# Optimization experiments

Hardware: AMD Instinct MI355X
Metric: run time of the kernel (lower is better)

The kernel has to match this reference:

```python
import jax, jax.numpy as jnp
import numpy as np


def setup_inputs() -> dict:
    key = jax.random.key(0)
    ks = jax.random.split(key, 4)
    B, T, C, L, DQ = 8, 2048, 256, 32, 512
    return {
        "vis_feats": jax.random.normal(ks[0], (B, T, C), dtype=jnp.float32),
        "query": jax.random.normal(ks[1], (B, L, DQ), dtype=jnp.float32),
        "W1": jax.random.normal(ks[2], (DQ, C), dtype=jnp.float32) / np.float32(np.sqrt(DQ)),
        "b1": jnp.zeros((C,), dtype=jnp.float32),
        "W2": jax.random.normal(ks[3], (DQ, C), dtype=jnp.float32) / np.float32(np.sqrt(DQ)),
        "b2": jnp.zeros((C,), dtype=jnp.float32),
        "window_size": 32,
        "num_chunks": 8,
    }


def reference(vis_feats, query, W1, b1, W2, b2, window_size, num_chunks):
    B, T, C = vis_feats.shape
    L = query.shape[1]
    # seq encoders (modeled as linear projections): [B, L, C]
    enc1 = query @ W1 + b1
    enc2 = query @ W2 + b2
    # clip-word similarity and per-clip word label: [B, T]
    sim = jnp.einsum("btc,blc->btl", vis_feats, enc1)
    clip_labels = jnp.argmax(sim, axis=2)
    NW = T - window_size + 1
    cic = window_size // num_chunks  # clips per chunk
    # sliding-window unfold indices: [NW, window_size]
    idx = jnp.arange(NW)[:, None] + jnp.arange(window_size)[None, :]
    vis_unf = vis_feats[:, idx, :]                      # [B, NW, W, C]
    lab_unf = clip_labels[:, idx].reshape(B, NW, num_chunks, cic)
    # majority vote per chunk == argmax of label histogram (ties -> smallest label,
    # matching np.bincount + np.argmax)
    counts = jax.nn.one_hot(lab_unf, L, dtype=jnp.int32).sum(axis=3)  # [B, NW, K, L]
    lbls = jnp.argmax(counts, axis=-1)                  # [B, NW, K]
    # adaptive_avg_pool3d (K, cic, C) -> (K, 1, C) == mean over clips-in-chunk
    pooled = vis_unf.reshape(B, NW, num_chunks, cic, C).mean(axis=3)  # [B, NW, K, C]
    # gather the majority-vote word encoding and modulate
    gathered = enc2[jnp.arange(B)[:, None, None], lbls]  # [B, NW, K, C]
    return gathered * pooled
```

## Files before the change

### kernel.cpp

```cpp
#include <hip/hip_runtime.h>
#include <hip/hip_bf16.h>

#define B   8
#define T   2048
#define C   256
#define L   32
#define DQ  512
#define NW  2017
#define NK  8
#define CIC 4
#define WT  32
#define SROWS (WT + (NK-1)*CIC)
#define LT  32

__global__ __launch_bounds__(256) void enc_kernel(
    const float* __restrict__ query, const float* __restrict__ W1,
    const float* __restrict__ b1, const float* __restrict__ W2,
    const float* __restrict__ b2, float* __restrict__ enc1,
    float* __restrict__ enc2) {
  const int b = blockIdx.y, lg = blockIdx.x;
  const int c = threadIdx.x;
  const float* q0 = query + ((size_t)b * L + lg * 4) * DQ;
  float a1[4] = {0.f, 0.f, 0.f, 0.f};
  float a2[4] = {0.f, 0.f, 0.f, 0.f};
#pragma unroll 8
  for (int d = 0; d < DQ; ++d) {
    const float w1 = W1[d * C + c];
    const float w2 = W2[d * C + c];
#pragma unroll
    for (int j = 0; j < 4; ++j) {
      const float qv = q0[j * DQ + d];
      a1[j] = fmaf(qv, w1, a1[j]);
      a2[j] = fmaf(qv, w2, a2[j]);
    }
  }
  const float bb1 = b1[c], bb2 = b2[c];
#pragma unroll
  for (int j = 0; j < 4; ++j) {
    const size_t off = ((size_t)b * L + lg * 4 + j) * C + c;
    enc1[off] = a1[j] + bb1;
    enc2[off] = a2[j] + bb2;
  }
}

__global__ __launch_bounds__(256) void label_kernel(
    const float* __restrict__ vis, const float* __restrict__ enc1,
    int* __restrict__ labels) {
  const int b = blockIdx.y;
  const int t0 = blockIdx.x * LT;
  const int tid = threadIdx.x;
  const int l = tid & 31;
  const int part = tid >> 5;
  __shared__ float4 raw[LT * (C / 4)];
  __shared__ alignas(16) float pacc[4][LT][36];

  float4 ef[8];
  {
    const float4* e1p = (const float4*)(enc1 + ((size_t)b * L + l) * C) + part * 8;
#pragma unroll
    for (int j = 0; j < 8; ++j) ef[j] = e1p[j];
  }
  const float4* vb = (const float4*)(vis + (size_t)b * T * C);
  for (int i = tid; i < LT * (C / 4); i += 256)
    raw[i] = vb[(size_t)(t0 + (i >> 6)) * (C / 4) + (i & 63)];
  __syncthreads();

  for (int t = 0; t < LT; ++t) {
    const float4* vr = &raw[t * (C / 4) + part * 8];
    float a = 0.f;
#pragma unroll
    for (int j = 0; j < 8; ++j) {
      const float4 v = vr[j];
      a = fmaf(v.x, ef[j].x, fmaf(v.y, ef[j].y, fmaf(v.z, ef[j].z, fmaf(v.w, ef[j].w, a))));
    }
    a += __shfl_down(a, 32);
    if (!(tid & 32)) pacc[tid >> 6][t][l] = a;
  }
  __syncthreads();

  if (tid < LT) {
    float4 s4[8];
#pragma unroll
    for (int j = 0; j < 8; ++j) s4[j] = make_float4(0.f, 0.f, 0.f, 0.f);
#pragma unroll
    for (int p = 0; p < 4; ++p) {
      const float4* pp = (const float4*)pacc[p][tid];
#pragma unroll
      for (int j = 0; j < 8; ++j) {
        s4[j].x += pp[j].x; s4[j].y += pp[j].y;
        s4[j].z += pp[j].z; s4[j].w += pp[j].w;
      }
    }
    float bv = -INFINITY;
    int bi = 0;
#pragma unroll
    for (int j = 0; j < 8; ++j) {
      if (s4[j].x > bv) { bv = s4[j].x; bi = 4 * j; }
      if (s4[j].y > bv) { bv = s4[j].y; bi = 4 * j + 1; }
      if (s4[j].z > bv) { bv = s4[j].z; bi = 4 * j + 2; }
      if (s4[j].w > bv) { bv = s4[j].w; bi = 4 * j + 3; }
    }
    labels[(size_t)b * T + t0 + tid] = bi;
  }
}

__global__ __launch_bounds__(256) void out_kernel(
    const float* __restrict__ vis, const float* __restrict__ enc2,
    const int* __restrict__ labels, float* __restrict__ out) {
  const int b = blockIdx.y;
  const int w0 = blockIdx.x * WT;
  const int tid = threadIdx.x;
  const int lane = tid & 63;
  const int wv = tid >> 6;
  __shared__ float4 S4[SROWS * (C / 4)];
  __shared__ int slbl[SROWS];

  int l0 = 0, l1 = 0, l2 = 0, l3 = 0;
  if (tid < SROWS) {
    const int* lb = labels + (size_t)b * T;
    const int t = w0 + tid;
#define LCL(tt) lb[(tt) > (T - 1) ? (T - 1) : (tt)]
    l0 = LCL(t); l1 = LCL(t + 1); l2 = LCL(t + 2); l3 = LCL(t + 3);
#undef LCL
  }

  const float4* vb = (const float4*)(vis + (size_t)b * T * C);
  float4 r[18];
  {
    const int s0 = wv * (SROWS / 4);
#pragma unroll
    for (int j = 0; j < 18; ++j) {
      int t = w0 + s0 + j;
      t = t > (T - 1) ? (T - 1) : t;
      r[j] = vb[(size_t)t * (C / 4) + lane];
    }
  }

  if (tid < SROWS) {
    const int c0 = 1 + (l0 == l1) + (l0 == l2) + (l0 == l3);
    const int c1 = 1 + (l1 == l0) + (l1 == l2) + (l1 == l3);
    const int c2 = 1 + (l2 == l0) + (l2 == l1) + (l2 == l3);
    const int c3 = 1 + (l3 == l0) + (l3 == l1) + (l3 == l2);
    int best = l0, bc = c0;
    if (c1 > bc || (c1 == bc && l1 < best)) { best = l1; bc = c1; }
    if (c2 > bc || (c2 == bc && l2 < best)) { best = l2; bc = c2; }
    if (c3 > bc || (c3 == bc && l3 < best)) { best = l3; bc = c3; }
    slbl[tid] = best;
  }

  {
    const int s0 = wv * (SROWS / 4);
#pragma unroll
    for (int s = 0; s < SROWS / 4; ++s) {
      float4 o;
      o.x = (r[s].x + r[s + 1].x + r[s + 2].x + r[s + 3].x) * 0.25f;
      o.y = (r[s].y + r[s + 1].y + r[s + 2].y + r[s + 3].y) * 0.25f;
      o.z = (r[s].z + r[s + 1].z + r[s + 2].z + r[s + 3].z) * 0.25f;
      o.w = (r[s].w + r[s + 1].w + r[s + 2].w + r[s + 3].w) * 0.25f;
      S4[(s0 + s) * (C / 4) + lane] = o;
    }
  }
  __syncthreads();

  const float4* e2b = (const float4*)(enc2 + (size_t)b * L * C);
  float4* outp = (float4*)out;
  const int wlim = (NW - w0) < WT ? (NW - w0) : WT;
#pragma unroll
  for (int kk = 0; kk < 2; ++kk) {
    const int k = wv + kk * 4;
#pragma unroll 4
    for (int w = 0; w < wlim; ++w) {
      const int s = w + CIC * k;
      const int lb = slbl[s];
      const float4 e = e2b[lb * (C / 4) + lane];
      const float4 sv = S4[s * (C / 4) + lane];
      float4 o;
      o.x = e.x * sv.x; o.y = e.y * sv.y; o.z = e.z * sv.z; o.w = e.w * sv.w;
      outp[(((size_t)b * NW + w0 + w) * NK + k) * (C / 4) + lane] = o;
    }
  }
}

extern "C" void kernel_launch(void* const* d_in, const int* in_sizes, int n_in,
                              void* d_out, int out_size, void* d_ws, size_t ws_size,
                              hipStream_t stream) {
  const float* vis   = (const float*)d_in[0];
  const float* query = (const float*)d_in[1];
  const float* W1    = (const float*)d_in[2];
  const float* b1    = (const float*)d_in[3];
  const float* W2    = (const float*)d_in[4];
  const float* b2    = (const float*)d_in[5];
  float* out = (float*)d_out;

  float* enc1 = (float*)d_ws;
  float* enc2 = enc1 + (size_t)B * L * C;
  int* labels = (int*)(enc2 + (size_t)B * L * C);

  enc_kernel<<<dim3(L / 4, B), 256, 0, stream>>>(query, W1, b1, W2, b2, enc1, enc2);
  label_kernel<<<dim3(T / LT, B), 256, 0, stream>>>(vis, enc1, labels);
  out_kernel<<<dim3((NW + WT - 1) / WT, B), 256, 0, stream>>>(vis, enc2, labels, out);
}
```

Measured before the change: 229.1 us.

## Split encoder projection over DQ into partial-sum blocks plus reduction kernel

```diff
diff --git a/kernel.cpp b/kernel.cpp
--- a/kernel.cpp
+++ b/kernel.cpp
@@ -12,34 +12,64 @@
 #define WT  32
 #define SROWS (WT + (NK-1)*CIC)
 #define LT  32
-
-__global__ __launch_bounds__(256) void enc_kernel(
+#define DS  4
+#define DSL (DQ / DS)
+#define PCHUNK (2 * B * L * C)
+
+__global__ __launch_bounds__(256) void enc_partial(
     const float* __restrict__ query, const float* __restrict__ W1,
-    const float* __restrict__ b1, const float* __restrict__ W2,
+    const float* __restrict__ W2, float* __restrict__ P) {
+  const int lg = blockIdx.x, b = blockIdx.y, ds = blockIdx.z;
+  const int c = threadIdx.x;
+  __shared__ float4 qs4[4][DSL / 4];
+
+  if (c < 4 * (DSL / 4)) {
+    const int j = c >> 5, g = c & 31;
+    qs4[j][g] = ((const float4*)(query + ((size_t)b * L + lg * 4 + j) * DQ + ds * DSL))[g];
+  }
+  __syncthreads();
+
+  float a1[4] = {0.f, 0.f, 0.f, 0.f};
+  float a2[4] = {0.f, 0.f, 0.f, 0.f};
+#pragma unroll 4
+  for (int g = 0; g < DSL / 4; ++g) {
+    const float4 q0 = qs4[0][g], q1 = qs4[1][g], q2 = qs4[2][g], q3 = qs4[3][g];
+    const float* wp1 = W1 + (size_t)(ds * DSL + 4 * g) * C + c;
+    const float* wp2 = W2 + (size_t)(ds * DSL + 4 * g) * C + c;
+    const float w10 = wp1[0], w11 = wp1[C], w12 = wp1[2 * C], w13 = wp1[3 * C];
+    const float w20 = wp2[0], w21 = wp2[C], w22 = wp2[2 * C], w23 = wp2[3 * C];
+    a1[0] = fmaf(q0.x, w10, fmaf(q0.y, w11, fmaf(q0.z, w12, fmaf(q0.w, w13, a1[0]))));
+    a1[1] = fmaf(q1.x, w10, fmaf(q1.y, w11, fmaf(q1.z, w12, fmaf(q1.w, w13, a1[1]))));
+    a1[2] = fmaf(q2.x, w10, fmaf(q2.y, w11, fmaf(q2.z, w12, fmaf(q2.w, w13, a1[2]))));
+    a1[3] = fmaf(q3.x, w10, fmaf(q3.y, w11, fmaf(q3.z, w12, fmaf(q3.w, w13, a1[3]))));
+    a2[0] = fmaf(q0.x, w20, fmaf(q0.y, w21, fmaf(q0.z, w22, fmaf(q0.w, w23, a2[0]))));
+    a2[1] = fmaf(q1.x, w20, fmaf(q1.y, w21, fmaf(q1.z, w22, fmaf(q1.w, w23, a2[1]))));
+    a2[2] = fmaf(q2.x, w20, fmaf(q2.y, w21, fmaf(q2.z, w22, fmaf(q2.w, w23, a2[2]))));
+    a2[3] = fmaf(q3.x, w20, fmaf(q3.y, w21, fmaf(q3.z, w22, fmaf(q3.w, w23, a2[3]))));
+  }
+
+#pragma unroll
+  for (int j = 0; j < 4; ++j) {
+    const size_t base = ((((size_t)ds * 2 + 0) * B + b) * 8 + lg) * 4 + j;
+    P[base * C + c] = a1[j];
+    P[(base + (size_t)B * 8 * 4) * C + c] = a2[j];
+  }
+}
+
+__global__ __launch_bounds__(256) void enc_reduce(
+    const float* __restrict__ P, const float* __restrict__ b1,
     const float* __restrict__ b2, float* __restrict__ enc1,
     float* __restrict__ enc2) {
-  const int b = blockIdx.y, lg = blockIdx.x;
-  const int c = threadIdx.x;
-  const float* q0 = query + ((size_t)b * L + lg * 4) * DQ;
-  float a1[4] = {0.f, 0.f, 0.f, 0.f};
-  float a2[4] = {0.f, 0.f, 0.f, 0.f};
-#pragma unroll 8
-  for (int d = 0; d < DQ; ++d) {
-    const float w1 = W1[d * C + c];
-    const float w2 = W2[d * C + c];
-#pragma unroll
-    for (int j = 0; j < 4; ++j) {
-      const float qv = q0[j * DQ + d];
-      a1[j] = fmaf(qv, w1, a1[j]);
-      a2[j] = fmaf(qv, w2, a2[j]);
-    }
-  }
-  const float bb1 = b1[c], bb2 = b2[c];
-#pragma unroll
-  for (int j = 0; j < 4; ++j) {
-    const size_t off = ((size_t)b * L + lg * 4 + j) * C + c;
-    enc1[off] = a1[j] + bb1;
-    enc2[off] = a2[j] + bb2;
+  const int tid = threadIdx.x;
+#pragma unroll
+  for (int k = 0; k < 8; ++k) {
+    const int idx = (blockIdx.x * 8 + k) * 256 + tid;
+    const float v = P[idx] + P[idx + PCHUNK] + P[idx + 2 * PCHUNK] + P[idx + 3 * PCHUNK];
+    const int e = idx >> 16;
+    const int r = idx & 65535;
+    const int cc = idx & 255;
+    if (e == 0) enc1[r] = v + b1[cc];
+    else        enc2[r] = v + b2[cc];
   }
 }
 
@@ -195,8 +225,10 @@
   float* enc1 = (float*)d_ws;
   float* enc2 = enc1 + (size_t)B * L * C;
   int* labels = (int*)(enc2 + (size_t)B * L * C);
-
-  enc_kernel<<<dim3(L / 4, B), 256, 0, stream>>>(query, W1, b1, W2, b2, enc1, enc2);
+  float* P = (float*)(labels + (size_t)B * T);
+
+  enc_partial<<<dim3(8, B, DS), 256, 0, stream>>>(query, W1, W2, P);
+  enc_reduce<<<64, 256, 0, stream>>>(P, b1, b2, enc1, enc2);
   label_kernel<<<dim3(T / LT, B), 256, 0, stream>>>(vis, enc1, labels);
   out_kernel<<<dim3((NW + WT - 1) / WT, B), 256, 0, stream>>>(vis, enc2, labels, out);
 }
```

Result: faster. 203.8 us (-11.0%).
